# Kernel optimization log

Hardware: AMD Instinct MI355X
Metric: run time of the kernel (lower is better)

## Reference

```python
import jax, jax.numpy as jnp
import numpy as np

# dims: T tokens, E experts, D model dim, F ffn dim, C per-expert capacity, K top-k routing
T, E, D, F, C, K = 4096, 8, 1024, 4096, 1536, 2


def setup_inputs() -> dict:
    key = jax.random.key(0)
    k_x, k_lg, k_w1, k_w2 = jax.random.split(key, 4)
    x = jax.random.normal(k_x, (T, D), jnp.float32)
    # external router: top-K of logits per token, softmax weights over kept logits
    logits = jax.random.normal(k_lg, (T, E), jnp.float32)
    topv, topi = jax.lax.top_k(logits, K)                      # (T,K)
    rows = jnp.arange(T)[:, None]
    route_mask = jnp.zeros((T, E), bool).at[rows, topi].set(True)
    route_weight = jnp.zeros((T, E), jnp.float32).at[rows, topi].set(
        jax.nn.softmax(topv, axis=-1))
    # stacked homogeneous expert MLP params (E leading axis, as in _stack_group)
    W1 = jax.random.normal(k_w1, (E, D, F), jnp.float32) / np.sqrt(D)
    b1 = jnp.zeros((E, F), jnp.float32)
    W2 = jax.random.normal(k_w2, (E, F, D), jnp.float32) / np.sqrt(F)
    b2 = jnp.zeros((E, D), jnp.float32)
    return dict(x=x, route_mask=route_mask, route_weight=route_weight,
                W1=W1, b1=b1, W2=W2, b2=b2)


def reference(x, route_mask, route_weight, W1, b1, W2, b2):
    """MoE with per-expert capacity: top-C tokens per expert by route weight,
    gather -> vmapped expert MLP -> weighted scatter-combine.
    Math identical to the one-hot slot einsums ('ect,t...->ec...' dispatch and
    'ecf,ect,te->tf' combine) of the original, expressed as gather/scatter.
    """
    Tn, En = route_mask.shape
    w_te = jnp.where(route_mask, route_weight, 0.0)            # (T,E)
    # per-expert scores; unrouted tokens get -inf so they can never be selected
    w_et = jnp.where(route_mask.T, w_te.T, -jnp.inf)           # (E,T)
    vals, idx = jax.lax.top_k(w_et, C)                         # (E,C) token ids per slot
    valid = jnp.isfinite(vals)                                  # slot actually filled
    # dispatch: gather token features into (E,C,D); empty slots are zero rows
    xe = x[idx] * valid[..., None]
    # grouped expert MLP (vmap over E via batched einsum)
    h = jax.nn.relu(jnp.einsum('ecd,edf->ecf', xe, W1) + b1[:, None, :])
    out = jnp.einsum('ecf,efd->ecd', h, W2) + b2[:, None, :]    # (E,C,D)
    # combine: y[t] = sum over slots assigned to t of w_te[t,e] * out[e,c]
    gain = jnp.where(valid, jnp.take_along_axis(w_te.T, idx, axis=1), 0.0)  # (E,C)
    y = jnp.zeros((Tn, out.shape[-1]), out.dtype)
    y = y.at[idx.reshape(-1)].add((out * gain[..., None]).reshape(-1, out.shape[-1]))
    return y
```

## Files before the change

### kernel.cpp

```cpp
#include <hip/hip_runtime.h>
#include <hip/hip_bf16.h>
#include <stdint.h>

#define T_TOK 4096
#define NE    8
#define DM    1024
#define FF    4096
#define CAP   1536

typedef __attribute__((ext_vector_type(8))) __bf16 bf16x8;
typedef __attribute__((ext_vector_type(4))) float  f32x4;

__device__ __forceinline__ void gload_lds16(const void* gptr, void* lptr) {
  __builtin_amdgcn_global_load_lds(
      (__attribute__((address_space(1))) void*)(uintptr_t)gptr,
      (__attribute__((address_space(3))) void*)(uintptr_t)lptr,
      16, 0, 0);
}


__global__ void conv_x_kernel(const float4* __restrict__ src, ushort4* __restrict__ dst, int n4) {
  int i = blockIdx.x * blockDim.x + threadIdx.x;
  if (i >= n4) return;
  float4 v = src[i];
  ushort4 o;
  o.x = __builtin_bit_cast(unsigned short, __float2bfloat16(v.x));
  o.y = __builtin_bit_cast(unsigned short, __float2bfloat16(v.y));
  o.z = __builtin_bit_cast(unsigned short, __float2bfloat16(v.z));
  o.w = __builtin_bit_cast(unsigned short, __float2bfloat16(v.w));
  dst[i] = o;
}

__global__ void tconv_kernel(const float* __restrict__ src, __hip_bfloat16* __restrict__ dst,
                             int R, int C) {
  __shared__ float tile[32][33];
  const int b  = blockIdx.z;
  const int r0 = blockIdx.y * 32;
  const int c0 = blockIdx.x * 32;
  const float* s = src + (size_t)b * R * C;
  __hip_bfloat16* d = dst + (size_t)b * R * C;
  const int tx = threadIdx.x, ty = threadIdx.y;
#pragma unroll
  for (int rr = ty; rr < 32; rr += 8)
    tile[rr][tx] = s[(size_t)(r0 + rr) * C + c0 + tx];
  __syncthreads();
#pragma unroll
  for (int cc = ty; cc < 32; cc += 8)
    d[(size_t)(c0 + cc) * R + r0 + tx] = __float2bfloat16(tile[tx][cc]);
}

__global__ void router_kernel(const float* __restrict__ rw, int* __restrict__ counts,
                              int* __restrict__ tok_ids, float* __restrict__ gains) {
  int t = blockIdx.x * blockDim.x + threadIdx.x;
  if (t >= T_TOK) return;
#pragma unroll
  for (int e = 0; e < NE; ++e) {
    float w = rw[t * NE + e];
    if (w > 0.f) {
      int pos = atomicAdd(&counts[e], 1);
      if (pos < CAP) {
        tok_ids[e * CAP + pos] = t;
        gains[e * CAP + pos]   = w;
      }
    }
  }
}

__global__ void pad_kernel(const int* __restrict__ counts, int* __restrict__ tok_ids,
                           float* __restrict__ gains) {
  int i = blockIdx.x * blockDim.x + threadIdx.x;
  if (i >= NE * CAP) return;
  int e = i / CAP, pos = i % CAP;
  int ne = min(counts[e], CAP);
  if (pos >= ne) { tok_ids[i] = 0; gains[i] = 0.f; }
}


template <int PASS>
__global__ __launch_bounds__(256, 2)
void moe_gemm(const __hip_bfloat16* __restrict__ Asrc,
              const __hip_bfloat16* __restrict__ Bsrc,
              const float* __restrict__ bias,
              const int* __restrict__ counts,
              const int* __restrict__ tok_ids,
              const float* __restrict__ gains,
              __hip_bfloat16* __restrict__ Hout,
              float* __restrict__ y)
{
  constexpr int K  = (PASS == 1) ? DM : FF;
  constexpr int NP = (PASS == 1) ? FF : DM;
  constexpr int MT = CAP / 128;
  constexpr int NT = NP / 128;

  const int bid = blockIdx.x;
  const int e   = bid / (MT * NT);
  const int rem = bid % (MT * NT);
  const int mt  = rem / NT;
  const int nt  = rem % NT;

  const int Ne = min(counts[e], CAP);
  const int m0 = mt * 128;
  if (m0 >= Ne) return;
  const int n0 = nt * 128;

  __shared__ alignas(16) __hip_bfloat16 As[128 * 32];
  __shared__ alignas(16) __hip_bfloat16 Bs[128 * 32];

  const int tid  = threadIdx.x;
  const int lane = tid & 63;
  const int wid  = tid >> 6;
  const int wm   = wid >> 1;
  const int wn   = wid & 1;

  const int srow0 = tid >> 2;
  const int srow1 = 64 + (tid >> 2);
  const int schk  = (tid & 3) * 8;

  const __hip_bfloat16 *aptr0, *aptr1;
  if (PASS == 1) {
    const int tok0 = tok_ids[e * CAP + m0 + srow0];
    const int tok1 = tok_ids[e * CAP + m0 + srow1];
    aptr0 = Asrc + (size_t)tok0 * DM + schk;
    aptr1 = Asrc + (size_t)tok1 * DM + schk;
  } else {
    aptr0 = Asrc + ((size_t)e * CAP + m0 + srow0) * FF + schk;
    aptr1 = Asrc + ((size_t)e * CAP + m0 + srow1) * FF + schk;
  }
  const __hip_bfloat16* bptr0 = Bsrc + ((size_t)e * NP + n0 + srow0) * K + schk;
  const __hip_bfloat16* bptr1 = Bsrc + ((size_t)e * NP + n0 + srow1) * K + schk;

  char* asw0 = (char*)As + wid * 1024;
  char* asw1 = (char*)As + 4096 + wid * 1024;
  char* bsw0 = (char*)Bs + wid * 1024;
  char* bsw1 = (char*)Bs + 4096 + wid * 1024;

  const char* AsB = (const char*)As;
  const char* BsB = (const char*)Bs;
  const int fr = lane & 15;
  const int fq = lane >> 4;
  const int koffB = fq * 16;

  f32x4 acc[4][4] = {};

  for (int k0 = 0; k0 < K; k0 += 32) {
    gload_lds16(aptr0, asw0);
    gload_lds16(aptr1, asw1);
    gload_lds16(bptr0, bsw0);
    gload_lds16(bptr1, bsw1);
    aptr0 += 32; aptr1 += 32; bptr0 += 32; bptr1 += 32;
    __syncthreads();

    bf16x8 af[4], bfr[4];
#pragma unroll
    for (int i = 0; i < 4; ++i)
      af[i] = *(const bf16x8*)(AsB + (wm * 64 + i * 16 + fr) * 64 + koffB);
#pragma unroll
    for (int j = 0; j < 4; ++j)
      bfr[j] = *(const bf16x8*)(BsB + (wn * 64 + j * 16 + fr) * 64 + koffB);
#pragma unroll
    for (int i = 0; i < 4; ++i)
#pragma unroll
      for (int j = 0; j < 4; ++j)
        acc[i][j] = __builtin_amdgcn_mfma_f32_16x16x32_bf16(af[i], bfr[j], acc[i][j], 0, 0, 0);
    __syncthreads();
  }

  const int colb = n0 + wn * 64 + fr;
  if (PASS == 1) {
#pragma unroll
    for (int j = 0; j < 4; ++j) {
      const float bv = bias[(size_t)e * NP + colb + j * 16];
#pragma unroll
      for (int i = 0; i < 4; ++i)
#pragma unroll
        for (int rr = 0; rr < 4; ++rr) {
          const int row = m0 + wm * 64 + i * 16 + fq * 4 + rr;
          float v = acc[i][j][rr] + bv;
          v = v > 0.f ? v : 0.f;
          Hout[((size_t)e * CAP + row) * FF + colb + j * 16] = __float2bfloat16(v);
        }
    }
  } else {
    float bv[4];
#pragma unroll
    for (int j = 0; j < 4; ++j) bv[j] = bias[(size_t)e * NP + colb + j * 16];
#pragma unroll
    for (int i = 0; i < 4; ++i)
#pragma unroll
      for (int rr = 0; rr < 4; ++rr) {
        const int row  = m0 + wm * 64 + i * 16 + fq * 4 + rr;
        const int slot = e * CAP + row;
        const float g  = gains[slot];
        if (g != 0.f) {
          const int tok = tok_ids[slot];
          float* yrow = y + (size_t)tok * DM + colb;
#pragma unroll
          for (int j = 0; j < 4; ++j)
            atomicAdd(yrow + j * 16, (acc[i][j][rr] + bv[j]) * g);
        }
      }
  }
}


extern "C" void kernel_launch(void* const* d_in, const int* in_sizes, int n_in,
                              void* d_out, int out_size, void* d_ws, size_t ws_size,
                              hipStream_t stream) {
  const float* x  = (const float*)d_in[0];
  const float* rw = (const float*)d_in[2];
  const float* W1 = (const float*)d_in[3];
  const float* b1 = (const float*)d_in[4];
  const float* W2 = (const float*)d_in[5];
  const float* b2 = (const float*)d_in[6];
  float* y = (float*)d_out;

  char* ws = (char*)d_ws;
  size_t off = 0;
  auto alloc = [&](size_t bytes) {
    void* p = ws + off;
    off = (off + bytes + 255) & ~(size_t)255;
    return p;
  };
  __hip_bfloat16* xb  = (__hip_bfloat16*)alloc((size_t)T_TOK * DM * 2);
  __hip_bfloat16* w1t = (__hip_bfloat16*)alloc((size_t)NE * DM * FF * 2);
  __hip_bfloat16* w2t = (__hip_bfloat16*)alloc((size_t)NE * FF * DM * 2);
  __hip_bfloat16* Hb  = (__hip_bfloat16*)alloc((size_t)NE * CAP * FF * 2);
  int*   counts  = (int*)alloc(NE * sizeof(int));
  int*   tok_ids = (int*)alloc((size_t)NE * CAP * sizeof(int));
  float* gains   = (float*)alloc((size_t)NE * CAP * sizeof(float));
  (void)ws_size; (void)in_sizes; (void)n_in; (void)out_size;

  hipMemsetAsync(y, 0, (size_t)T_TOK * DM * sizeof(float), stream);
  hipMemsetAsync(counts, 0, NE * sizeof(int), stream);

  conv_x_kernel<<<(T_TOK * DM / 4 + 255) / 256, 256, 0, stream>>>(
      (const float4*)x, (ushort4*)xb, T_TOK * DM / 4);
  tconv_kernel<<<dim3(FF / 32, DM / 32, NE), dim3(32, 8), 0, stream>>>(W1, w1t, DM, FF);
  tconv_kernel<<<dim3(DM / 32, FF / 32, NE), dim3(32, 8), 0, stream>>>(W2, w2t, FF, DM);
  router_kernel<<<(T_TOK + 255) / 256, 256, 0, stream>>>(rw, counts, tok_ids, gains);
  pad_kernel<<<(NE * CAP + 255) / 256, 256, 0, stream>>>(counts, tok_ids, gains);

  moe_gemm<1><<<NE * (CAP / 128) * (FF / 128), 256, 0, stream>>>(
      xb, w1t, b1, counts, tok_ids, gains, Hb, nullptr);
  moe_gemm<2><<<NE * (CAP / 128) * (DM / 128), 256, 0, stream>>>(
      Hb, w2t, b2, counts, tok_ids, gains, nullptr, y);
}
```

Baseline: 390.2 us.

## Add split-K to second GEMM, swizzle LDS, remap blocks, widen transpose tiles

```diff
diff --git a/kernel.cpp b/kernel.cpp
--- a/kernel.cpp
+++ b/kernel.cpp
@@ -31,22 +31,34 @@
   dst[i] = o;
 }
 
-__global__ void tconv_kernel(const float* __restrict__ src, __hip_bfloat16* __restrict__ dst,
-                             int R, int C) {
-  __shared__ float tile[32][33];
+__global__ __launch_bounds__(256)
+void tconv_kernel(const float* __restrict__ src, __hip_bfloat16* __restrict__ dst,
+                  int R, int C) {
+  __shared__ float tile[64][65];
   const int b  = blockIdx.z;
-  const int r0 = blockIdx.y * 32;
-  const int c0 = blockIdx.x * 32;
+  const int r0 = blockIdx.y * 64;
+  const int c0 = blockIdx.x * 64;
   const float* s = src + (size_t)b * R * C;
   __hip_bfloat16* d = dst + (size_t)b * R * C;
-  const int tx = threadIdx.x, ty = threadIdx.y;
-#pragma unroll
-  for (int rr = ty; rr < 32; rr += 8)
+  const int tid = threadIdx.x;
+  const int tx = tid & 63, ty = tid >> 6;
+#pragma unroll
+  for (int rr = ty; rr < 64; rr += 4)
     tile[rr][tx] = s[(size_t)(r0 + rr) * C + c0 + tx];
   __syncthreads();
-#pragma unroll
-  for (int cc = ty; cc < 32; cc += 8)
-    d[(size_t)(c0 + cc) * R + r0 + tx] = __float2bfloat16(tile[tx][cc]);
+  const int lg = tid & 15;
+  const int cg = tid >> 4;
+#pragma unroll
+  for (int w = 0; w < 4; ++w) {
+    const int cc = w * 16 + cg;
+    const int r4 = lg * 4;
+    ushort4 o;
+    o.x = __builtin_bit_cast(unsigned short, __float2bfloat16(tile[r4 + 0][cc]));
+    o.y = __builtin_bit_cast(unsigned short, __float2bfloat16(tile[r4 + 1][cc]));
+    o.z = __builtin_bit_cast(unsigned short, __float2bfloat16(tile[r4 + 2][cc]));
+    o.w = __builtin_bit_cast(unsigned short, __float2bfloat16(tile[r4 + 3][cc]));
+    *(ushort4*)&d[(size_t)(c0 + cc) * R + r0 + r4] = o;
+  }
 }
 
 __global__ void router_kernel(const float* __restrict__ rw, int* __restrict__ counts,
@@ -76,32 +88,38 @@
 }
 
 
-template <int PASS>
-__global__ __launch_bounds__(256, 2)
-void moe_gemm(const __hip_bfloat16* __restrict__ Asrc,
-              const __hip_bfloat16* __restrict__ Bsrc,
-              const float* __restrict__ bias,
-              const int* __restrict__ counts,
-              const int* __restrict__ tok_ids,
-              const float* __restrict__ gains,
-              __hip_bfloat16* __restrict__ Hout,
-              float* __restrict__ y)
+template <int PASS, int SK>
+__global__ __launch_bounds__(256, 4)
+void moe_gemm97(const __hip_bfloat16* __restrict__ Asrc,
+                const __hip_bfloat16* __restrict__ Bsrc,
+                const float* __restrict__ bias,
+                const int* __restrict__ counts,
+                const int* __restrict__ tok_ids,
+                const float* __restrict__ gains,
+                __hip_bfloat16* __restrict__ Hout,
+                float* __restrict__ y)
 {
-  constexpr int K  = (PASS == 1) ? DM : FF;
-  constexpr int NP = (PASS == 1) ? FF : DM;
-  constexpr int MT = CAP / 128;
-  constexpr int NT = NP / 128;
-
-  const int bid = blockIdx.x;
-  const int e   = bid / (MT * NT);
-  const int rem = bid % (MT * NT);
-  const int mt  = rem / NT;
-  const int nt  = rem % NT;
+  constexpr int K   = (PASS == 1) ? DM : FF;
+  constexpr int NP  = (PASS == 1) ? FF : DM;
+  constexpr int MT  = CAP / 128;
+  constexpr int NT  = NP / 128;
+  constexpr int KP  = K / SK;
+  constexpr int KT  = KP / 32;
+  constexpr int NWG = NE * MT * NT * SK;
+
+  const int id = (blockIdx.x & 7) * (NWG / 8) + (blockIdx.x >> 3);
+  const int e  = id / (SK * NT * MT);
+  int r        = id % (SK * NT * MT);
+  const int sp = r / (NT * MT);
+  r            = r % (NT * MT);
+  const int nt = r / MT;
+  const int mt = r % MT;
 
   const int Ne = min(counts[e], CAP);
   const int m0 = mt * 128;
   if (m0 >= Ne) return;
   const int n0 = nt * 128;
+  const int k0 = sp * KP;
 
   __shared__ alignas(16) __hip_bfloat16 As[128 * 32];
   __shared__ alignas(16) __hip_bfloat16 Bs[128 * 32];
@@ -112,51 +130,44 @@
   const int wm   = wid >> 1;
   const int wn   = wid & 1;
 
-  const int srow0 = tid >> 2;
-  const int srow1 = 64 + (tid >> 2);
-  const int schk  = (tid & 3) * 8;
+  const int srow = tid >> 2;
+  const int cs   = ((tid & 3) ^ ((srow >> 1) & 3)) * 8;
 
   const __hip_bfloat16 *aptr0, *aptr1;
   if (PASS == 1) {
-    const int tok0 = tok_ids[e * CAP + m0 + srow0];
-    const int tok1 = tok_ids[e * CAP + m0 + srow1];
-    aptr0 = Asrc + (size_t)tok0 * DM + schk;
-    aptr1 = Asrc + (size_t)tok1 * DM + schk;
+    const int tok0 = tok_ids[e * CAP + m0 + srow];
+    const int tok1 = tok_ids[e * CAP + m0 + 64 + srow];
+    aptr0 = Asrc + (size_t)tok0 * DM + k0 + cs;
+    aptr1 = Asrc + (size_t)tok1 * DM + k0 + cs;
   } else {
-    aptr0 = Asrc + ((size_t)e * CAP + m0 + srow0) * FF + schk;
-    aptr1 = Asrc + ((size_t)e * CAP + m0 + srow1) * FF + schk;
-  }
-  const __hip_bfloat16* bptr0 = Bsrc + ((size_t)e * NP + n0 + srow0) * K + schk;
-  const __hip_bfloat16* bptr1 = Bsrc + ((size_t)e * NP + n0 + srow1) * K + schk;
-
-  char* asw0 = (char*)As + wid * 1024;
-  char* asw1 = (char*)As + 4096 + wid * 1024;
-  char* bsw0 = (char*)Bs + wid * 1024;
-  char* bsw1 = (char*)Bs + 4096 + wid * 1024;
+    aptr0 = Asrc + ((size_t)e * CAP + m0 + srow) * FF + k0 + cs;
+    aptr1 = Asrc + ((size_t)e * CAP + m0 + 64 + srow) * FF + k0 + cs;
+  }
+  const __hip_bfloat16* bptr0 = Bsrc + (((size_t)e * NP + n0 + srow) * K) + k0 + cs;
+  const __hip_bfloat16* bptr1 = Bsrc + (((size_t)e * NP + n0 + 64 + srow) * K) + k0 + cs;
 
   const char* AsB = (const char*)As;
   const char* BsB = (const char*)Bs;
   const int fr = lane & 15;
   const int fq = lane >> 4;
-  const int koffB = fq * 16;
+  const int kbyte = ((fq ^ ((fr >> 1) & 3)) << 4);
 
   f32x4 acc[4][4] = {};
 
-  for (int k0 = 0; k0 < K; k0 += 32) {
-    gload_lds16(aptr0, asw0);
-    gload_lds16(aptr1, asw1);
-    gload_lds16(bptr0, bsw0);
-    gload_lds16(bptr1, bsw1);
-    aptr0 += 32; aptr1 += 32; bptr0 += 32; bptr1 += 32;
+  for (int kt = 0; kt < KT; ++kt) {
+    gload_lds16(aptr0 + kt * 32, (char*)As + wid * 1024);
+    gload_lds16(aptr1 + kt * 32, (char*)As + 4096 + wid * 1024);
+    gload_lds16(bptr0 + kt * 32, (char*)Bs + wid * 1024);
+    gload_lds16(bptr1 + kt * 32, (char*)Bs + 4096 + wid * 1024);
     __syncthreads();
 
     bf16x8 af[4], bfr[4];
 #pragma unroll
     for (int i = 0; i < 4; ++i)
-      af[i] = *(const bf16x8*)(AsB + (wm * 64 + i * 16 + fr) * 64 + koffB);
+      af[i] = *(const bf16x8*)(AsB + (wm * 64 + i * 16 + fr) * 64 + kbyte);
 #pragma unroll
     for (int j = 0; j < 4; ++j)
-      bfr[j] = *(const bf16x8*)(BsB + (wn * 64 + j * 16 + fr) * 64 + koffB);
+      bfr[j] = *(const bf16x8*)(BsB + (wn * 64 + j * 16 + fr) * 64 + kbyte);
 #pragma unroll
     for (int i = 0; i < 4; ++i)
 #pragma unroll
@@ -183,7 +194,8 @@
   } else {
     float bv[4];
 #pragma unroll
-    for (int j = 0; j < 4; ++j) bv[j] = bias[(size_t)e * NP + colb + j * 16];
+    for (int j = 0; j < 4; ++j)
+      bv[j] = (sp == 0) ? bias[(size_t)e * NP + colb + j * 16] : 0.f;
 #pragma unroll
     for (int i = 0; i < 4; ++i)
 #pragma unroll
@@ -235,13 +247,13 @@
 
   conv_x_kernel<<<(T_TOK * DM / 4 + 255) / 256, 256, 0, stream>>>(
       (const float4*)x, (ushort4*)xb, T_TOK * DM / 4);
-  tconv_kernel<<<dim3(FF / 32, DM / 32, NE), dim3(32, 8), 0, stream>>>(W1, w1t, DM, FF);
-  tconv_kernel<<<dim3(DM / 32, FF / 32, NE), dim3(32, 8), 0, stream>>>(W2, w2t, FF, DM);
+  tconv_kernel<<<dim3(FF / 64, DM / 64, NE), 256, 0, stream>>>(W1, w1t, DM, FF);
+  tconv_kernel<<<dim3(DM / 64, FF / 64, NE), 256, 0, stream>>>(W2, w2t, FF, DM);
   router_kernel<<<(T_TOK + 255) / 256, 256, 0, stream>>>(rw, counts, tok_ids, gains);
   pad_kernel<<<(NE * CAP + 255) / 256, 256, 0, stream>>>(counts, tok_ids, gains);
 
-  moe_gemm<1><<<NE * (CAP / 128) * (FF / 128), 256, 0, stream>>>(
+  moe_gemm97<1, 1><<<NE * (CAP / 128) * (FF / 128) * 1, 256, 0, stream>>>(
       xb, w1t, b1, counts, tok_ids, gains, Hb, nullptr);
-  moe_gemm<2><<<NE * (CAP / 128) * (DM / 128), 256, 0, stream>>>(
+  moe_gemm97<2, 4><<<NE * (CAP / 128) * (DM / 128) * 4, 256, 0, stream>>>(
       Hb, w2t, b2, counts, tok_ids, gains, nullptr, y);
 }
```

After: 388.4 us. No clear change (-0.5%).
